# Optimization experiments

Measured on AMD Instinct MI355X. Metric: run time of the kernel, lower is better.

Reference implementation:

```python
import jax, jax.numpy as jnp
import numpy as np

B, N, H, W = 8, 128, 128, 128


def setup_inputs() -> dict:
    key = jax.random.key(0)
    k1, k2, k3 = jax.random.split(key, 3)
    logit = jax.random.normal(k1, (B, N, H, W), dtype=jnp.float32)
    target = jax.random.randint(k2, (B, H, W), 0, N, dtype=jnp.int64)
    weight = jax.random.uniform(k3, (B, N), dtype=jnp.float32)
    return {"logit": logit, "target": target, "weight": weight, "epoch": 1}


def reference(logit, target, weight, epoch):
    # Seesaw loss (weight branch). p = 1, C = ones, reduction = 'mean'.
    exp = jnp.exp(logit)  # [B, N, H, W]
    # Mitigation matrix M[b, i, j] = (w_i / w_j)**p if w_i > w_j else 1
    wi = weight[:, :, None]  # [B, N, 1]
    wj = weight[:, None, :]  # [B, 1, N]
    M = jnp.where(wi > wj, wi / wj, jnp.float32(1.0))  # [B, N, N]
    # numerator: exp at the target class per pixel -> [B, H, W]
    num = jnp.take_along_axis(exp, target[:, None, :, :], axis=1)[:, 0]
    # tmp_c[b, j, h, w] = sum_i exp[b, i, h, w] * M[b, i, j]  (C is all ones)
    denom = jnp.einsum("bihw,bij->bjhw", exp, M)  # [B, N, H, W]
    denom_t = jnp.take_along_axis(denom, target[:, None, :, :], axis=1)[:, 0]
    log = -jnp.log(num / denom_t)  # [B, H, W]
    return log.mean()
```

## Files before the change

### kernel.cpp

```cpp
#include <hip/hip_runtime.h>


#define B_   8
#define N_   128
#define HW_  16384
#define BLOCK 256
#define BLOCKS_PER_B (HW_ / BLOCK)
#define NBLOCKS (B_ * BLOCKS_PER_B)
#define NPIX (B_ * HW_)

__global__ __launch_bounds__(BLOCK) void seesaw_main(
    const float* __restrict__ logit,
    const int*   __restrict__ target,
    const float* __restrict__ weight,
    float*       __restrict__ partials)
{
    __shared__ float w_s[N_];
    __shared__ float red[BLOCK / 64];

    const int b   = blockIdx.x / BLOCKS_PER_B;
    const int pix = (blockIdx.x % BLOCKS_PER_B) * BLOCK + threadIdx.x;

    if (threadIdx.x < N_) w_s[threadIdx.x] = weight[b * N_ + threadIdx.x];
    __syncthreads();

    const int   t      = target[b * HW_ + pix];
    const float wt     = w_s[t];
    const float inv_wt = 1.0f / wt;

    const float* lp = logit + (size_t)b * N_ * HW_ + pix;

    float acc = 0.0f;
    float lt  = 0.0f;

    #pragma unroll 8
    for (int i = 0; i < N_; ++i) {
        const float l  = lp[(size_t)i * HW_];
        const float e  = __expf(l);
        const float wi = w_s[i];
        const float m  = (wi > wt) ? wi * inv_wt : 1.0f;
        acc = fmaf(e, m, acc);
        if (i == t) lt = l;
    }

    float loss = __logf(acc) - lt;

    #pragma unroll
    for (int o = 32; o > 0; o >>= 1) loss += __shfl_down(loss, o, 64);

    const int lane = threadIdx.x & 63;
    const int wid  = threadIdx.x >> 6;
    if (lane == 0) red[wid] = loss;
    __syncthreads();

    if (threadIdx.x == 0) {
        float s = 0.0f;
        #pragma unroll
        for (int k = 0; k < BLOCK / 64; ++k) s += red[k];
        partials[blockIdx.x] = s;
    }
}

__global__ __launch_bounds__(256) void seesaw_reduce(
    const float* __restrict__ partials,
    float*       __restrict__ out)
{
    __shared__ float red[4];
    float s = partials[threadIdx.x] + partials[threadIdx.x + 256];

    #pragma unroll
    for (int o = 32; o > 0; o >>= 1) s += __shfl_down(s, o, 64);

    const int lane = threadIdx.x & 63;
    const int wid  = threadIdx.x >> 6;
    if (lane == 0) red[wid] = s;
    __syncthreads();

    if (threadIdx.x == 0) {
        float tot = red[0] + red[1] + red[2] + red[3];
        out[0] = tot / (float)NPIX;
    }
}

extern "C" void kernel_launch(void* const* d_in, const int* in_sizes, int n_in,
                              void* d_out, int out_size, void* d_ws, size_t ws_size,
                              hipStream_t stream)
{
    const float* logit  = (const float*)d_in[0];
    const int*   target = (const int*)  d_in[1];
    const float* weight = (const float*)d_in[2];

    float* partials = (float*)d_ws;
    float* out      = (float*)d_out;

    seesaw_main<<<NBLOCKS, BLOCK, 0, stream>>>(logit, target, weight, partials);
    seesaw_reduce<<<1, 256, 0, stream>>>(partials, out);
}
```

Before: 20.34 us.

## Vectorize pixel loads with four pixels per thread and simplify mitigation via max

Each thread now processes four adjacent pixels using float4 logit loads and an int4 target load, with 64-thread blocks. The per-class mitigation factor is rewritten as max(w_i, w_t), and the division by w_t is moved into a log subtraction at the end, removing the branch and the reciprocal. The block-level shared reduction is replaced by a single wave shuffle, and the final reduce runs with 512 threads. The aim is fewer, wider memory transactions and less ALU work per element, at the cost of far fewer waves in flight to hide latency.

```diff
diff --git a/kernel.cpp b/kernel.cpp
--- a/kernel.cpp
+++ b/kernel.cpp
@@ -1,13 +1,15 @@
 #include <hip/hip_runtime.h>
 
 
-#define B_   8
-#define N_   128
-#define HW_  16384
-#define BLOCK 256
-#define BLOCKS_PER_B (HW_ / BLOCK)
+#define B_    8
+#define N_    128
+#define HW_   16384
+#define NPIX  (B_ * HW_)
+#define BLOCK 64
+#define PPT   4
+#define PIX_PER_BLOCK (BLOCK * PPT)
+#define BLOCKS_PER_B  (HW_ / PIX_PER_BLOCK)
 #define NBLOCKS (B_ * BLOCKS_PER_B)
-#define NPIX (B_ * HW_)
 
 __global__ __launch_bounds__(BLOCK) void seesaw_main(
     const float* __restrict__ logit,
@@ -16,57 +18,55 @@
     float*       __restrict__ partials)
 {
     __shared__ float w_s[N_];
-    __shared__ float red[BLOCK / 64];
 
-    const int b   = blockIdx.x / BLOCKS_PER_B;
-    const int pix = (blockIdx.x % BLOCKS_PER_B) * BLOCK + threadIdx.x;
+    const int b    = blockIdx.x >> 6;
+    const int pix0 = (blockIdx.x & 63) * PIX_PER_BLOCK + threadIdx.x * PPT;
 
-    if (threadIdx.x < N_) w_s[threadIdx.x] = weight[b * N_ + threadIdx.x];
+    w_s[threadIdx.x]      = weight[b * N_ + threadIdx.x];
+    w_s[threadIdx.x + 64] = weight[b * N_ + threadIdx.x + 64];
     __syncthreads();
 
-    const int   t      = target[b * HW_ + pix];
-    const float wt     = w_s[t];
-    const float inv_wt = 1.0f / wt;
+    const int4 t4 = *(const int4*)(target + b * HW_ + pix0);
 
-    const float* lp = logit + (size_t)b * N_ * HW_ + pix;
+    const float wt0 = w_s[t4.x], wt1 = w_s[t4.y], wt2 = w_s[t4.z], wt3 = w_s[t4.w];
+    const float lw0 = __logf(wt0), lw1 = __logf(wt1), lw2 = __logf(wt2), lw3 = __logf(wt3);
 
-    float acc = 0.0f;
-    float lt  = 0.0f;
+    const float* lp = logit + (size_t)b * N_ * HW_ + pix0;
 
-    #pragma unroll 8
+    float a0 = 0.f, a1 = 0.f, a2 = 0.f, a3 = 0.f;
+    float l0 = 0.f, l1 = 0.f, l2 = 0.f, l3 = 0.f;
+
+    #pragma unroll 16
     for (int i = 0; i < N_; ++i) {
-        const float l  = lp[(size_t)i * HW_];
-        const float e  = __expf(l);
+        const float4 l = *(const float4*)(lp + (size_t)i * HW_);
         const float wi = w_s[i];
-        const float m  = (wi > wt) ? wi * inv_wt : 1.0f;
-        acc = fmaf(e, m, acc);
-        if (i == t) lt = l;
+        a0 = fmaf(__expf(l.x), fmaxf(wi, wt0), a0);
+        a1 = fmaf(__expf(l.y), fmaxf(wi, wt1), a1);
+        a2 = fmaf(__expf(l.z), fmaxf(wi, wt2), a2);
+        a3 = fmaf(__expf(l.w), fmaxf(wi, wt3), a3);
+        l0 = (i == t4.x) ? l.x : l0;
+        l1 = (i == t4.y) ? l.y : l1;
+        l2 = (i == t4.z) ? l.z : l2;
+        l3 = (i == t4.w) ? l.w : l3;
     }
 
-    float loss = __logf(acc) - lt;
+    float loss = (__logf(a0) - lw0 - l0)
+               + (__logf(a1) - lw1 - l1)
+               + (__logf(a2) - lw2 - l2)
+               + (__logf(a3) - lw3 - l3);
 
     #pragma unroll
     for (int o = 32; o > 0; o >>= 1) loss += __shfl_down(loss, o, 64);
 
-    const int lane = threadIdx.x & 63;
-    const int wid  = threadIdx.x >> 6;
-    if (lane == 0) red[wid] = loss;
-    __syncthreads();
-
-    if (threadIdx.x == 0) {
-        float s = 0.0f;
-        #pragma unroll
-        for (int k = 0; k < BLOCK / 64; ++k) s += red[k];
-        partials[blockIdx.x] = s;
-    }
+    if (threadIdx.x == 0) partials[blockIdx.x] = loss;
 }
 
-__global__ __launch_bounds__(256) void seesaw_reduce(
+__global__ __launch_bounds__(512) void seesaw_reduce(
     const float* __restrict__ partials,
     float*       __restrict__ out)
 {
-    __shared__ float red[4];
-    float s = partials[threadIdx.x] + partials[threadIdx.x + 256];
+    __shared__ float red[8];
+    float s = partials[threadIdx.x];
 
     #pragma unroll
     for (int o = 32; o > 0; o >>= 1) s += __shfl_down(s, o, 64);
@@ -77,8 +77,10 @@
     __syncthreads();
 
     if (threadIdx.x == 0) {
-        float tot = red[0] + red[1] + red[2] + red[3];
-        out[0] = tot / (float)NPIX;
+        float tot = 0.f;
+        #pragma unroll
+        for (int k = 0; k < 8; ++k) tot += red[k];
+        out[0] = tot * (1.0f / (float)NPIX);
     }
 }
 
@@ -94,5 +96,5 @@
     float* out      = (float*)d_out;
 
     seesaw_main<<<NBLOCKS, BLOCK, 0, stream>>>(logit, target, weight, partials);
-    seesaw_reduce<<<1, 256, 0, stream>>>(partials, out);
+    seesaw_reduce<<<1, 512, 0, stream>>>(partials, out);
 }
```

New measurement: 23.68 us. 1.16x slower.

## Split class loop across two thread halves and simplify mitigation factor algebraically

Applied to the files above, without the earlier changes.

Each block now covers 128 pixels with 256 threads, and each half of the block sums over 64 of the 128 classes. The partial sums are combined through shared memory, which doubles the number of blocks and cuts the serial loop length per thread to raise memory-level parallelism. The mitigation factor is rewritten as max(wi, wt) with log(wt) subtracted once at the end, which removes the per-iteration compare and select. The reduce kernel is widened to 1024 threads to match the 1024 partials, and the extra sync and half-idle threads in the epilogue add some overhead.

```diff
diff --git a/kernel.cpp b/kernel.cpp
--- a/kernel.cpp
+++ b/kernel.cpp
@@ -1,13 +1,15 @@
 #include <hip/hip_runtime.h>
 
 
-#define B_   8
-#define N_   128
-#define HW_  16384
+#define B_    8
+#define N_    128
+#define HALF_N 64
+#define HW_   16384
+#define NPIX  (B_ * HW_)
 #define BLOCK 256
-#define BLOCKS_PER_B (HW_ / BLOCK)
+#define PIX_PER_BLOCK 128
+#define BLOCKS_PER_B  (HW_ / PIX_PER_BLOCK)
 #define NBLOCKS (B_ * BLOCKS_PER_B)
-#define NPIX (B_ * HW_)
 
 __global__ __launch_bounds__(BLOCK) void seesaw_main(
     const float* __restrict__ logit,
@@ -16,34 +18,44 @@
     float*       __restrict__ partials)
 {
     __shared__ float w_s[N_];
+    __shared__ float sa[PIX_PER_BLOCK];
+    __shared__ float sl[PIX_PER_BLOCK];
     __shared__ float red[BLOCK / 64];
 
-    const int b   = blockIdx.x / BLOCKS_PER_B;
-    const int pix = (blockIdx.x % BLOCKS_PER_B) * BLOCK + threadIdx.x;
+    const int b    = blockIdx.x >> 7;
+    const int pl   = threadIdx.x & 127;
+    const int half = threadIdx.x >> 7;
+    const int pix  = (blockIdx.x & 127) * PIX_PER_BLOCK + pl;
 
     if (threadIdx.x < N_) w_s[threadIdx.x] = weight[b * N_ + threadIdx.x];
     __syncthreads();
 
-    const int   t      = target[b * HW_ + pix];
-    const float wt     = w_s[t];
-    const float inv_wt = 1.0f / wt;
+    const int   t  = target[b * HW_ + pix];
+    const float wt = w_s[t];
 
-    const float* lp = logit + (size_t)b * N_ * HW_ + pix;
+    const float* lp = logit + (size_t)b * N_ * HW_ + (size_t)half * HALF_N * HW_ + pix;
+    const int ibase = half * HALF_N;
 
-    float acc = 0.0f;
-    float lt  = 0.0f;
+    float a  = 0.0f;
+    float lt = 0.0f;
 
-    #pragma unroll 8
-    for (int i = 0; i < N_; ++i) {
-        const float l  = lp[(size_t)i * HW_];
-        const float e  = __expf(l);
-        const float wi = w_s[i];
-        const float m  = (wi > wt) ? wi * inv_wt : 1.0f;
-        acc = fmaf(e, m, acc);
-        if (i == t) lt = l;
+    #pragma unroll 16
+    for (int k = 0; k < HALF_N; ++k) {
+        const float l  = lp[(size_t)k * HW_];
+        const float wi = w_s[ibase + k];
+        a  = fmaf(__expf(l), fmaxf(wi, wt), a);
+        lt = (ibase + k == t) ? l : lt;
     }
 
-    float loss = __logf(acc) - lt;
+    if (half) { sa[pl] = a; sl[pl] = lt; }
+    __syncthreads();
+
+    float loss = 0.0f;
+    if (!half) {
+        const float at = a + sa[pl];
+        const float lf = lt + sl[pl];
+        loss = __logf(at) - __logf(wt) - lf;
+    }
 
     #pragma unroll
     for (int o = 32; o > 0; o >>= 1) loss += __shfl_down(loss, o, 64);
@@ -61,12 +73,12 @@
     }
 }
 
-__global__ __launch_bounds__(256) void seesaw_reduce(
+__global__ __launch_bounds__(1024) void seesaw_reduce(
     const float* __restrict__ partials,
     float*       __restrict__ out)
 {
-    __shared__ float red[4];
-    float s = partials[threadIdx.x] + partials[threadIdx.x + 256];
+    __shared__ float red[16];
+    float s = partials[threadIdx.x];
 
     #pragma unroll
     for (int o = 32; o > 0; o >>= 1) s += __shfl_down(s, o, 64);
@@ -77,8 +89,10 @@
     __syncthreads();
 
     if (threadIdx.x == 0) {
-        float tot = red[0] + red[1] + red[2] + red[3];
-        out[0] = tot / (float)NPIX;
+        float tot = 0.0f;
+        #pragma unroll
+        for (int k = 0; k < 16; ++k) tot += red[k];
+        out[0] = tot * (1.0f / (float)NPIX);
     }
 }
 
@@ -94,5 +108,5 @@
     float* out      = (float*)d_out;
 
     seesaw_main<<<NBLOCKS, BLOCK, 0, stream>>>(logit, target, weight, partials);
-    seesaw_reduce<<<1, 256, 0, stream>>>(partials, out);
+    seesaw_reduce<<<1, 1024, 0, stream>>>(partials, out);
 }
```

Result: faster. 18.40 us (-9.5%).
